# Kernel tuning notes

Hardware: AMD Instinct MI355X
Metric: run time of the kernel (lower is better)

Reference implementation:

```python
import jax, jax.numpy as jnp
import numpy as np
import math

D_MODEL = 1024
N_HEADS = 16
D_HEAD = D_MODEL // N_HEADS
D_FF = 4096
BATCH = 2
SEQ = 2048
EPS = 1e-5


def _rmsnorm(x, w):
    rms = jnp.sqrt(jnp.mean(x * x, axis=-1, keepdims=True) + EPS)
    return (x / rms) * w


def _gelu_erf(x):
    # matches 0.5 * x * (1 + erf(x / sqrt(2)))
    return 0.5 * x * (1.0 + jax.lax.erf(x / jnp.sqrt(jnp.asarray(2.0, x.dtype))))


def setup_inputs() -> dict:
    key = jax.random.key(0)
    ks = jax.random.split(key, 6)
    scale = 0.02
    x = jax.random.normal(ks[0], (BATCH, SEQ, D_MODEL), dtype=jnp.float32)
    w_qkv = jax.random.normal(ks[1], (3 * D_MODEL, D_MODEL), dtype=jnp.float32) * scale
    w_o = jax.random.normal(ks[2], (D_MODEL, D_MODEL), dtype=jnp.float32) * scale
    ln1_w = jnp.ones((D_MODEL,), dtype=jnp.float32)
    ln2_w = jnp.ones((D_MODEL,), dtype=jnp.float32)
    w1 = jax.random.normal(ks[3], (D_FF, D_MODEL), dtype=jnp.float32) * scale
    w2 = jax.random.normal(ks[4], (D_MODEL, D_FF), dtype=jnp.float32) * scale
    return {"x": x, "w_qkv": w_qkv, "w_o": w_o, "ln1_w": ln1_w,
            "ln2_w": ln2_w, "w1": w1, "w2": w2}


def reference(x, w_qkv, w_o, ln1_w, ln2_w, w1, w2):
    B, S, D = x.shape
    # --- attention sublayer (pre-norm) ---
    h = _rmsnorm(x, ln1_w)
    qkv = jnp.einsum('bsd,ed->bse', h, w_qkv)            # (B,S,3*D)
    qkv = qkv.reshape(B, S, 3, N_HEADS, D_HEAD)
    q, k, v = jnp.moveaxis(qkv, 2, 0)                    # each (B,S,H,dh)
    q = q.transpose(0, 2, 1, 3)                          # (B,H,S,dh)
    k = k.transpose(0, 2, 1, 3)
    v = v.transpose(0, 2, 1, 3)
    scores = jnp.einsum('bhqd,bhkd->bhqk', q, k) / math.sqrt(D_HEAD)
    causal = jnp.tril(jnp.ones((S, S), dtype=bool))      # True = keep
    scores = jnp.where(causal, scores, jnp.asarray(-jnp.inf, scores.dtype))
    attn = jax.nn.softmax(scores, axis=-1)
    ctx = jnp.einsum('bhqk,bhkd->bhqd', attn, v)         # (B,H,S,dh)
    ctx = ctx.transpose(0, 2, 1, 3).reshape(B, S, D)
    attn_out = jnp.einsum('bsd,ed->bse', ctx, w_o)
    first_sum = x + attn_out
    # --- FFN sublayer (pre-norm) ---
    h2 = _rmsnorm(first_sum, ln2_w)
    ff = jnp.einsum('bsf,df->bsd', _gelu_erf(jnp.einsum('bsd,fd->bsf', h2, w1)), w2)
    return first_sum + ff
```

## Files before the change

kernel.cpp:

```cpp
#include <hip/hip_runtime.h>

typedef unsigned short u16;
typedef unsigned int u32;
typedef __attribute__((ext_vector_type(8))) short short8;
typedef __attribute__((ext_vector_type(4))) float f32x4;

#define AS1 __attribute__((address_space(1)))
#define AS3 __attribute__((address_space(3)))

__device__ __forceinline__ u16 f2bf(float f) {
  union { float f; unsigned u; } v; v.f = f;
  return (u16)((v.u + 0x7fffu + ((v.u >> 16) & 1u)) >> 16);
}
__device__ __forceinline__ u32 pack2bf(float a, float b) {
  return (u32)f2bf(a) | ((u32)f2bf(b) << 16);
}
__device__ __forceinline__ u32 permpack(float a, float b) {
  union { float f; u32 u; } ua, ub; ua.f = a; ub.f = b;
  return __builtin_amdgcn_perm(ub.u, ua.u, 0x07060302u);
}

__global__ void cvt_all_kernel(const float* __restrict__ wqkv, const float* __restrict__ wo,
                               const float* __restrict__ w1, const float* __restrict__ w2,
                               u16* __restrict__ oqkv, u16* __restrict__ oo,
                               u16* __restrict__ o1, u16* __restrict__ o2) {
  const int blk = blockIdx.x;
  const float* src; u16* dst; float scale = 1.0f; int off;
  if (blk < 3072) {
    src = wqkv; dst = oqkv; off = blk;
    if (blk >= 1024 && blk < 2048) scale = 0.125f;
  } else if (blk < 4096) {
    src = wo; dst = oo; off = blk - 3072;
  } else if (blk < 8192) {
    src = w1; dst = o1; off = blk - 4096;
  } else {
    src = w2; dst = o2; off = blk - 8192;
  }
  size_t i = ((size_t)off * 256 + threadIdx.x) * 4;
  float4 v = *(const float4*)(src + i);
  ushort4 o = make_ushort4(f2bf(v.x * scale), f2bf(v.y * scale),
                           f2bf(v.z * scale), f2bf(v.w * scale));
  *(ushort4*)(dst + i) = o;
}

__global__ void rmsnorm_kernel(const float* __restrict__ x, const float* __restrict__ w,
                               u16* __restrict__ out) {
  const int row = blockIdx.x, tid = threadIdx.x;
  const float4 v = ((const float4*)(x + (size_t)row * 1024))[tid];
  float ss = v.x * v.x + v.y * v.y + v.z * v.z + v.w * v.w;
#pragma unroll
  for (int off = 32; off > 0; off >>= 1) ss += __shfl_xor(ss, off);
  __shared__ float red[4];
  if ((tid & 63) == 0) red[tid >> 6] = ss;
  __syncthreads();
  float tot = red[0] + red[1] + red[2] + red[3];
  float scale = 1.0f / sqrtf(tot * (1.0f / 1024.0f) + 1e-5f);
  const float4 wv = ((const float4*)w)[tid];
  ushort4 o = make_ushort4(f2bf(v.x * scale * wv.x), f2bf(v.y * scale * wv.y),
                           f2bf(v.z * scale * wv.z), f2bf(v.w * scale * wv.w));
  ((ushort4*)(out + (size_t)row * 1024))[tid] = o;
}

template <int EPI>
__global__ __launch_bounds__(256, 4)
void gemm_bt(const u16* __restrict__ A, const u16* __restrict__ B,
             const float* __restrict__ RES, void* __restrict__ OUT,
             int M, int N, int K, int KS) {
  __shared__ __align__(16) u16 As[2][128 * 32];
  __shared__ __align__(16) u16 Bs[2][128 * 32];
  const int tid = threadIdx.x;
  const int wave = tid >> 6, lane = tid & 63;
  const int quad = lane >> 4, l16 = lane & 15;
  const int m0 = blockIdx.y * 128, n0 = blockIdx.x * 128;
  const int wm = (wave >> 1) * 64, wn = (wave & 1) * 64;
  f32x4 acc[4][4] = {};

  const int c0 = wave * 128 + lane;
  const int r0_row = c0 >> 2, r0_col = (c0 & 3) * 8;
  const int c1 = c0 + 64;
  const int r1_row = c1 >> 2, r1_col = (c1 & 3) * 8;

  const u16* ga0 = A + (size_t)(m0 + r0_row) * K + r0_col;
  const u16* ga1 = A + (size_t)(m0 + r1_row) * K + r1_col;
  const u16* gb0 = B + (size_t)(n0 + r0_row) * K + r0_col;
  const u16* gb1 = B + (size_t)(n0 + r1_row) * K + r1_col;

  const int kbeg = blockIdx.z * KS, kend = kbeg + KS;

  auto stage = [&](int k0, int pp) {
    __builtin_amdgcn_global_load_lds((AS1 void*)(ga0 + k0), (AS3 void*)(&As[pp][wave * 1024]), 16, 0, 0);
    __builtin_amdgcn_global_load_lds((AS1 void*)(ga1 + k0), (AS3 void*)(&As[pp][wave * 1024 + 512]), 16, 0, 0);
    __builtin_amdgcn_global_load_lds((AS1 void*)(gb0 + k0), (AS3 void*)(&Bs[pp][wave * 1024]), 16, 0, 0);
    __builtin_amdgcn_global_load_lds((AS1 void*)(gb1 + k0), (AS3 void*)(&Bs[pp][wave * 1024 + 512]), 16, 0, 0);
  };

  stage(kbeg, 0);
  int p = 0;
  for (int k0 = kbeg; k0 < kend; k0 += 32) {
    __syncthreads();
    if (k0 + 32 < kend) stage(k0 + 32, p ^ 1);
    short8 af[4], bfr[4];
#pragma unroll
    for (int i = 0; i < 4; ++i) {
      af[i]  = *(const short8*)(&As[p][(wm + i * 16 + l16) * 32 + quad * 8]);
      bfr[i] = *(const short8*)(&Bs[p][(wn + i * 16 + l16) * 32 + quad * 8]);
    }
#pragma unroll
    for (int i = 0; i < 4; ++i)
#pragma unroll
      for (int j = 0; j < 4; ++j)
        acc[i][j] = __builtin_amdgcn_mfma_f32_16x16x32_bf16(af[i], bfr[j], acc[i][j], 0, 0, 0);
    p ^= 1;
  }

  const size_t zoff = (size_t)blockIdx.z * M * N;
#pragma unroll
  for (int i = 0; i < 4; ++i) {
#pragma unroll
    for (int j = 0; j < 4; ++j) {
#pragma unroll
      for (int r = 0; r < 4; ++r) {
        int row = m0 + wm + i * 16 + quad * 4 + r;
        int col = n0 + wn + j * 16 + l16;
        size_t idx = (size_t)row * N + col;
        float v = acc[i][j][r];
        if constexpr (EPI == 0) {
          ((u16*)OUT)[idx] = f2bf(v);
        } else if constexpr (EPI == 1) {
          ((float*)OUT)[idx] = RES[idx] + v;
        } else if constexpr (EPI == 2) {
          float g = 0.5f * v * (1.0f + erff(v * 0.70710678118654752f));
          ((u16*)OUT)[idx] = f2bf(g);
        } else {
          ((float*)OUT)[zoff + idx] = v;
        }
      }
    }
  }
}

__global__ void reduce4_kernel(const float* __restrict__ fs,
                               const float* __restrict__ P,
                               float* __restrict__ out, size_t n) {
  size_t i = ((size_t)blockIdx.x * 256 + threadIdx.x) * 4;
  float4 a = *(const float4*)(fs + i);
  float4 p0 = *(const float4*)(P + i);
  float4 p1 = *(const float4*)(P + n + i);
  float4 p2 = *(const float4*)(P + 2 * n + i);
  float4 p3 = *(const float4*)(P + 3 * n + i);
  float4 o = make_float4(a.x + ((p0.x + p1.x) + (p2.x + p3.x)),
                         a.y + ((p0.y + p1.y) + (p2.y + p3.y)),
                         a.z + ((p0.z + p1.z) + (p2.z + p3.z)),
                         a.w + ((p0.w + p1.w) + (p2.w + p3.w)));
  *(float4*)(out + i) = o;
}

__global__ __launch_bounds__(256)
void packkv_kernel(const u16* __restrict__ qkv, u16* __restrict__ Kp,
                   u16* __restrict__ Vp) {
  __shared__ __align__(16) u16 Ks[32][72];
  __shared__ __align__(16) u16 Vs[32][72];
  const int kt = blockIdx.x, h = blockIdx.y, b = blockIdx.z;
  const int tid = threadIdx.x;
  const int key0 = kt * 32;
  {
    const size_t g = (size_t)b * 2048 * 3072 + (size_t)(key0 + (tid >> 3)) * 3072
                     + h * 64 + (tid & 7) * 8;
    *(short8*)(&Ks[tid >> 3][(tid & 7) * 8]) = *(const short8*)(qkv + g + 1024);
    *(short8*)(&Vs[tid >> 3][(tid & 7) * 8]) = *(const short8*)(qkv + g + 2048);
  }
  __syncthreads();
  const int wave = tid >> 6, lane = tid & 63;
  const int quad = lane >> 4, l16 = lane & 15;
  const int permrow = 8 * (l16 >> 2) + (l16 & 3);
  const size_t obase = ((size_t)((b * 16 + h) * 64 + kt)) * 2048 + tid * 8;
  {
    int row = permrow + (wave >> 1) * 4;
    int col = quad * 8 + (wave & 1) * 32;
    *(short8*)(Kp + obase) = *(const short8*)(&Ks[row][col]);
  }
  {
    short8 v;
    int col = wave * 16 + l16;
#pragma unroll
    for (int j = 0; j < 8; ++j) v[j] = (short)Vs[quad * 8 + j][col];
    *(short8*)(Vp + obase) = v;
  }
}

struct AttnState {
  f32x4 o0, o1, o2, o3;
  float ls;
};

template <bool MASKED>
__device__ __forceinline__ void attn_tile(
    AttnState& st, const u16* kp, const u16* vp, int key0, int q_abs, int quad,
    short8 qf0, short8 qf1) {
  short8 kf00 = *(const short8*)kp;
  short8 kf01 = *(const short8*)(kp + 512);
  short8 kf10 = *(const short8*)(kp + 1024);
  short8 kf11 = *(const short8*)(kp + 1536);
  short8 vf0 = *(const short8*)vp;
  short8 vf1 = *(const short8*)(vp + 512);
  short8 vf2 = *(const short8*)(vp + 1024);
  short8 vf3 = *(const short8*)(vp + 1536);

  f32x4 s0 = {}, s1 = {};
  s0 = __builtin_amdgcn_mfma_f32_16x16x32_bf16(kf00, qf0, s0, 0, 0, 0);
  s0 = __builtin_amdgcn_mfma_f32_16x16x32_bf16(kf01, qf1, s0, 0, 0, 0);
  s1 = __builtin_amdgcn_mfma_f32_16x16x32_bf16(kf10, qf0, s1, 0, 0, 0);
  s1 = __builtin_amdgcn_mfma_f32_16x16x32_bf16(kf11, qf1, s1, 0, 0, 0);

  float p[8];
#pragma unroll
  for (int r = 0; r < 4; ++r) {
    p[r]     = __expf(s0[r]);
    p[4 + r] = __expf(s1[r]);
  }
  if constexpr (MASKED) {
    const int kb = key0 + 8 * quad;
#pragma unroll
    for (int r = 0; r < 4; ++r) {
      if (kb + r > q_abs)     p[r] = 0.f;
      if (kb + 4 + r > q_abs) p[4 + r] = 0.f;
    }
  }
  st.ls += ((p[0] + p[1]) + (p[2] + p[3])) + ((p[4] + p[5]) + (p[6] + p[7]));

  union { u32 u[4]; short8 s; } pu;
  pu.u[0] = permpack(p[0], p[1]);
  pu.u[1] = permpack(p[2], p[3]);
  pu.u[2] = permpack(p[4], p[5]);
  pu.u[3] = permpack(p[6], p[7]);

  st.o0 = __builtin_amdgcn_mfma_f32_16x16x32_bf16(vf0, pu.s, st.o0, 0, 0, 0);
  st.o1 = __builtin_amdgcn_mfma_f32_16x16x32_bf16(vf1, pu.s, st.o1, 0, 0, 0);
  st.o2 = __builtin_amdgcn_mfma_f32_16x16x32_bf16(vf2, pu.s, st.o2, 0, 0, 0);
  st.o3 = __builtin_amdgcn_mfma_f32_16x16x32_bf16(vf3, pu.s, st.o3, 0, 0, 0);
}

__global__ __launch_bounds__(256)
void attn_kernel(const u16* __restrict__ qkv, const u16* __restrict__ Kpack,
                 const u16* __restrict__ Vpack, u16* __restrict__ ctx) {
  const int bx = blockIdx.x, by = blockIdx.y, bz = blockIdx.z;
  const int h = by, b = bz;
  const int qt = ((by >> 3) & 1) ? (31 - bx) : bx;
  const int tid = threadIdx.x, wave = tid >> 6, lane = tid & 63;
  const int quad = lane >> 4, l16 = lane & 15;
  const int q0 = qt * 64;
  const int qrow = q0 + wave * 16;
  const int q_abs = qrow + l16;
  const size_t base = (size_t)b * 2048 * 3072;
  const size_t headoff = (size_t)((b * 16 + h) * 64) * 2048;
  const u16* Kb = Kpack + headoff + lane * 8;
  const u16* Vb = Vpack + headoff + lane * 8;

  short8 qf0, qf1;
  {
    const u16* qp = qkv + base + (size_t)q_abs * 3072 + h * 64 + quad * 8;
    qf0 = *(const short8*)qp;
    qf1 = *(const short8*)(qp + 32);
  }
  AttnState st;
  st.o0 = f32x4{}; st.o1 = f32x4{}; st.o2 = f32x4{}; st.o3 = f32x4{};
  st.ls = 0.f;

  const int nfull = qrow >> 5;
  for (int kt = 0; kt < nfull; ++kt)
    attn_tile<false>(st, Kb + kt * 2048, Vb + kt * 2048, kt * 32, q_abs, quad, qf0, qf1);
  attn_tile<true>(st, Kb + nfull * 2048, Vb + nfull * 2048, nfull * 32, q_abs, quad, qf0, qf1);

  float ls = st.ls;
  ls += __shfl_xor(ls, 16);
  ls += __shfl_xor(ls, 32);
  float inv = 1.0f / ls;

  f32x4 o[4] = {st.o0, st.o1, st.o2, st.o3};
  u16* cp = ctx + (size_t)(b * 2048 + q_abs) * 1024 + h * 64 + quad * 4;
#pragma unroll
  for (int c = 0; c < 4; ++c) {
    u32 lo = pack2bf(o[c][0] * inv, o[c][1] * inv);
    u32 hi = pack2bf(o[c][2] * inv, o[c][3] * inv);
    *(uint2*)(cp + c * 16) = make_uint2(lo, hi);
  }
}

extern "C" void kernel_launch(void* const* d_in, const int* in_sizes, int n_in,
                              void* d_out, int out_size, void* d_ws, size_t ws_size,
                              hipStream_t stream) {
  const float* x     = (const float*)d_in[0];
  const float* w_qkv = (const float*)d_in[1];
  const float* w_o   = (const float*)d_in[2];
  const float* ln1   = (const float*)d_in[3];
  const float* ln2   = (const float*)d_in[4];
  const float* w1    = (const float*)d_in[5];
  const float* w2    = (const float*)d_in[6];
  float* out = (float*)d_out;

  char* p = (char*)d_ws;
  u16* wqkv_b = (u16*)p; p += (size_t)3072 * 1024 * 2;
  u16* wo_b   = (u16*)p; p += (size_t)1024 * 1024 * 2;
  u16* w1_b   = (u16*)p; p += (size_t)4096 * 1024 * 2;
  u16* w2_b   = (u16*)p; p += (size_t)1024 * 4096 * 2;
  u16* h_b    = (u16*)p; p += (size_t)4096 * 1024 * 2;
  u16* qkv_b  = (u16*)p;
  u16* g_b    = qkv_b;
  p += (size_t)4096 * 3072 * 2;
  u16* ctx_b  = (u16*)p; p += (size_t)4096 * 1024 * 2;
  float* fs   = (float*)p; p += (size_t)4096 * 1024 * 4;
  u16* kp_b   = (u16*)fs;
  u16* vp_b   = (u16*)fs + (size_t)4 * 1024 * 1024;
  float* Pbuf = (float*)p;
  const size_t need = (size_t)(p - (char*)d_ws) + (size_t)4 * 4096 * 1024 * 4;
  const bool splitk = ws_size >= need;

  cvt_all_kernel<<<12288, 256, 0, stream>>>(w_qkv, w_o, w1, w2,
                                            wqkv_b, wo_b, w1_b, w2_b);

  rmsnorm_kernel<<<4096, 256, 0, stream>>>(x, ln1, h_b);
  gemm_bt<0><<<dim3(24, 32, 1), 256, 0, stream>>>(h_b, wqkv_b, nullptr, qkv_b, 4096, 3072, 1024, 1024);
  packkv_kernel<<<dim3(64, 16, 2), 256, 0, stream>>>(qkv_b, kp_b, vp_b);
  attn_kernel<<<dim3(32, 16, 2), 256, 0, stream>>>(qkv_b, kp_b, vp_b, ctx_b);
  gemm_bt<1><<<dim3(8, 32, 1), 256, 0, stream>>>(ctx_b, wo_b, x, fs, 4096, 1024, 1024, 1024);
  rmsnorm_kernel<<<4096, 256, 0, stream>>>(fs, ln2, h_b);
  gemm_bt<2><<<dim3(32, 32, 1), 256, 0, stream>>>(h_b, w1_b, nullptr, g_b, 4096, 4096, 1024, 1024);
  if (splitk) {
    gemm_bt<3><<<dim3(8, 32, 4), 256, 0, stream>>>(g_b, w2_b, nullptr, Pbuf, 4096, 1024, 4096, 1024);
    reduce4_kernel<<<4096, 256, 0, stream>>>(fs, Pbuf, out, (size_t)4096 * 1024);
  } else {
    gemm_bt<1><<<dim3(8, 32, 1), 256, 0, stream>>>(g_b, w2_b, fs, out, 4096, 1024, 4096, 4096);
  }
}
```

Before: 356.7 us.

## Pre-pack weights into MFMA fragment layout and load B directly to registers

The weight conversion kernel now writes bf16 weights in a tiled layout matching the MFMA B-fragment order. The GEMM reads B straight from global memory into registers with one-step prefetch, so the B shared-memory buffers are gone. Split-K partials are also stored as bf16 instead of fp32, which halves partial-buffer traffic but loses some precision before the reduction. Launch bounds drop to 3 blocks per SM to fit the extra registers. The new packing kernel uses scalar, strided float loads that may be slower than the old vectorised conversion.

```diff
diff --git a/kernel.cpp b/kernel.cpp
--- a/kernel.cpp
+++ b/kernel.cpp
@@ -15,32 +15,45 @@
 __device__ __forceinline__ u32 pack2bf(float a, float b) {
   return (u32)f2bf(a) | ((u32)f2bf(b) << 16);
 }
+__device__ __forceinline__ float bf2f(u16 h) {
+  union { u32 u; float f; } v; v.u = ((u32)h) << 16; return v.f;
+}
 __device__ __forceinline__ u32 permpack(float a, float b) {
   union { float f; u32 u; } ua, ub; ua.f = a; ub.f = b;
   return __builtin_amdgcn_perm(ub.u, ua.u, 0x07060302u);
 }
 
-__global__ void cvt_all_kernel(const float* __restrict__ wqkv, const float* __restrict__ wo,
-                               const float* __restrict__ w1, const float* __restrict__ w2,
-                               u16* __restrict__ oqkv, u16* __restrict__ oo,
-                               u16* __restrict__ o1, u16* __restrict__ o2) {
-  const int blk = blockIdx.x;
-  const float* src; u16* dst; float scale = 1.0f; int off;
-  if (blk < 3072) {
-    src = wqkv; dst = oqkv; off = blk;
-    if (blk >= 1024 && blk < 2048) scale = 0.125f;
-  } else if (blk < 4096) {
-    src = wo; dst = oo; off = blk - 3072;
-  } else if (blk < 8192) {
-    src = w1; dst = o1; off = blk - 4096;
-  } else {
-    src = w2; dst = o2; off = blk - 8192;
-  }
-  size_t i = ((size_t)off * 256 + threadIdx.x) * 4;
-  float4 v = *(const float4*)(src + i);
-  ushort4 o = make_ushort4(f2bf(v.x * scale), f2bf(v.y * scale),
-                           f2bf(v.z * scale), f2bf(v.w * scale));
-  *(ushort4*)(dst + i) = o;
+__global__ __launch_bounds__(256)
+void packb_kernel(const float* __restrict__ wqkv, const float* __restrict__ wo,
+                  const float* __restrict__ w1, const float* __restrict__ w2,
+                  u16* __restrict__ oqkv, u16* __restrict__ oo,
+                  u16* __restrict__ o1, u16* __restrict__ o2) {
+  __shared__ u16 Ls[128][40];
+  const int b = blockIdx.x, t = threadIdx.x;
+  const float* W; u16* O; int nb, kb, KB; float scale = 1.0f;
+  if (b < 768)       { W = wqkv; O = oqkv; KB = 32;  int i2 = b;        nb = i2 >> 5; kb = i2 & 31;
+                       if (nb >= 8 && nb < 16) scale = 0.125f; }
+  else if (b < 1024) { W = wo;   O = oo;   KB = 32;  int i2 = b - 768;  nb = i2 >> 5; kb = i2 & 31; }
+  else if (b < 2048) { W = w1;   O = o1;   KB = 32;  int i2 = b - 1024; nb = i2 >> 5; kb = i2 & 31; }
+  else               { W = w2;   O = o2;   KB = 128; int i2 = b - 2048; nb = i2 >> 7; kb = i2 & 127; }
+  const int K = KB * 32;
+  {
+    const int r = t >> 1, c0 = (t & 1) * 16;
+    const float* src = W + (size_t)(nb * 128 + r) * K + kb * 32 + c0;
+#pragma unroll
+    for (int e = 0; e < 16; ++e) Ls[r][c0 + e] = f2bf(src[e] * scale);
+  }
+  __syncthreads();
+  const int f = t >> 5, l0 = (t & 31) * 2;
+  u16* dst = O + ((size_t)(nb * KB + kb) * 8 + f) * 512 + (size_t)l0 * 8;
+  short8 v0, v1;
+#pragma unroll
+  for (int e = 0; e < 8; ++e) v0[e] = (short)Ls[f * 16 + (l0 & 15)][(l0 >> 4) * 8 + e];
+  const int l1 = l0 + 1;
+#pragma unroll
+  for (int e = 0; e < 8; ++e) v1[e] = (short)Ls[f * 16 + (l1 & 15)][(l1 >> 4) * 8 + e];
+  *(short8*)dst = v0;
+  *(short8*)(dst + 8) = v1;
 }
 
 __global__ void rmsnorm_kernel(const float* __restrict__ x, const float* __restrict__ w,
@@ -62,16 +75,15 @@
 }
 
 template <int EPI>
-__global__ __launch_bounds__(256, 4)
-void gemm_bt(const u16* __restrict__ A, const u16* __restrict__ B,
+__global__ __launch_bounds__(256, 3)
+void gemm_bt(const u16* __restrict__ A, const u16* __restrict__ Bp,
              const float* __restrict__ RES, void* __restrict__ OUT,
              int M, int N, int K, int KS) {
   __shared__ __align__(16) u16 As[2][128 * 32];
-  __shared__ __align__(16) u16 Bs[2][128 * 32];
   const int tid = threadIdx.x;
   const int wave = tid >> 6, lane = tid & 63;
   const int quad = lane >> 4, l16 = lane & 15;
-  const int m0 = blockIdx.y * 128, n0 = blockIdx.x * 128;
+  const int m0 = blockIdx.y * 128;
   const int wm = (wave >> 1) * 64, wn = (wave & 1) * 64;
   f32x4 acc[4][4] = {};
 
@@ -79,40 +91,54 @@
   const int r0_row = c0 >> 2, r0_col = (c0 & 3) * 8;
   const int c1 = c0 + 64;
   const int r1_row = c1 >> 2, r1_col = (c1 & 3) * 8;
-
   const u16* ga0 = A + (size_t)(m0 + r0_row) * K + r0_col;
   const u16* ga1 = A + (size_t)(m0 + r1_row) * K + r1_col;
-  const u16* gb0 = B + (size_t)(n0 + r0_row) * K + r0_col;
-  const u16* gb1 = B + (size_t)(n0 + r1_row) * K + r1_col;
+
+  const u16* Bw = Bp + (((size_t)blockIdx.x * (K >> 5)) * 8 + (wave & 1) * 4) * 512
+                  + (size_t)lane * 8;
 
   const int kbeg = blockIdx.z * KS, kend = kbeg + KS;
 
   auto stage = [&](int k0, int pp) {
     __builtin_amdgcn_global_load_lds((AS1 void*)(ga0 + k0), (AS3 void*)(&As[pp][wave * 1024]), 16, 0, 0);
     __builtin_amdgcn_global_load_lds((AS1 void*)(ga1 + k0), (AS3 void*)(&As[pp][wave * 1024 + 512]), 16, 0, 0);
-    __builtin_amdgcn_global_load_lds((AS1 void*)(gb0 + k0), (AS3 void*)(&Bs[pp][wave * 1024]), 16, 0, 0);
-    __builtin_amdgcn_global_load_lds((AS1 void*)(gb1 + k0), (AS3 void*)(&Bs[pp][wave * 1024 + 512]), 16, 0, 0);
   };
 
   stage(kbeg, 0);
+  short8 bfr[4];
+  {
+    const u16* bp = Bw + (size_t)(kbeg >> 5) * 4096;
+#pragma unroll
+    for (int j = 0; j < 4; ++j) bfr[j] = *(const short8*)(bp + j * 512);
+  }
   int p = 0;
   for (int k0 = kbeg; k0 < kend; k0 += 32) {
     __syncthreads();
-    if (k0 + 32 < kend) stage(k0 + 32, p ^ 1);
-    short8 af[4], bfr[4];
-#pragma unroll
-    for (int i = 0; i < 4; ++i) {
-      af[i]  = *(const short8*)(&As[p][(wm + i * 16 + l16) * 32 + quad * 8]);
-      bfr[i] = *(const short8*)(&Bs[p][(wn + i * 16 + l16) * 32 + quad * 8]);
+    const bool more = (k0 + 32 < kend);
+    if (more) stage(k0 + 32, p ^ 1);
+    short8 bnext[4];
+    if (more) {
+      const u16* bp = Bw + (size_t)((k0 + 32) >> 5) * 4096;
+#pragma unroll
+      for (int j = 0; j < 4; ++j) bnext[j] = *(const short8*)(bp + j * 512);
     }
+    short8 af[4];
+#pragma unroll
+    for (int i = 0; i < 4; ++i)
+      af[i] = *(const short8*)(&As[p][(wm + i * 16 + l16) * 32 + quad * 8]);
 #pragma unroll
     for (int i = 0; i < 4; ++i)
 #pragma unroll
       for (int j = 0; j < 4; ++j)
         acc[i][j] = __builtin_amdgcn_mfma_f32_16x16x32_bf16(af[i], bfr[j], acc[i][j], 0, 0, 0);
+    if (more) {
+#pragma unroll
+      for (int j = 0; j < 4; ++j) bfr[j] = bnext[j];
+    }
     p ^= 1;
   }
 
+  const int n0 = blockIdx.x * 128;
   const size_t zoff = (size_t)blockIdx.z * M * N;
 #pragma unroll
   for (int i = 0; i < 4; ++i) {
@@ -132,7 +158,7 @@
           float g = 0.5f * v * (1.0f + erff(v * 0.70710678118654752f));
           ((u16*)OUT)[idx] = f2bf(g);
         } else {
-          ((float*)OUT)[zoff + idx] = v;
+          ((u16*)OUT)[zoff + idx] = f2bf(v);
         }
       }
     }
@@ -140,19 +166,17 @@
 }
 
 __global__ void reduce4_kernel(const float* __restrict__ fs,
-                               const float* __restrict__ P,
+                               const u16* __restrict__ P,
                                float* __restrict__ out, size_t n) {
   size_t i = ((size_t)blockIdx.x * 256 + threadIdx.x) * 4;
   float4 a = *(const float4*)(fs + i);
-  float4 p0 = *(const float4*)(P + i);
-  float4 p1 = *(const float4*)(P + n + i);
-  float4 p2 = *(const float4*)(P + 2 * n + i);
-  float4 p3 = *(const float4*)(P + 3 * n + i);
-  float4 o = make_float4(a.x + ((p0.x + p1.x) + (p2.x + p3.x)),
-                         a.y + ((p0.y + p1.y) + (p2.y + p3.y)),
-                         a.z + ((p0.z + p1.z) + (p2.z + p3.z)),
-                         a.w + ((p0.w + p1.w) + (p2.w + p3.w)));
-  *(float4*)(out + i) = o;
+  float s[4] = {a.x, a.y, a.z, a.w};
+#pragma unroll
+  for (int z = 0; z < 4; ++z) {
+    ushort4 q = *(const ushort4*)(P + z * n + i);
+    s[0] += bf2f(q.x); s[1] += bf2f(q.y); s[2] += bf2f(q.z); s[3] += bf2f(q.w);
+  }
+  *(float4*)(out + i) = make_float4(s[0], s[1], s[2], s[3]);
 }
 
 __global__ __launch_bounds__(256)
@@ -311,12 +335,12 @@
   float* fs   = (float*)p; p += (size_t)4096 * 1024 * 4;
   u16* kp_b   = (u16*)fs;
   u16* vp_b   = (u16*)fs + (size_t)4 * 1024 * 1024;
-  float* Pbuf = (float*)p;
-  const size_t need = (size_t)(p - (char*)d_ws) + (size_t)4 * 4096 * 1024 * 4;
+  u16* Pbuf = (u16*)p;
+  const size_t need = (size_t)(p - (char*)d_ws) + (size_t)4 * 4096 * 1024 * 2;
   const bool splitk = ws_size >= need;
 
-  cvt_all_kernel<<<12288, 256, 0, stream>>>(w_qkv, w_o, w1, w2,
-                                            wqkv_b, wo_b, w1_b, w2_b);
+  packb_kernel<<<3072, 256, 0, stream>>>(w_qkv, w_o, w1, w2,
+                                         wqkv_b, wo_b, w1_b, w2_b);
 
   rmsnorm_kernel<<<4096, 256, 0, stream>>>(x, ln1, h_b);
   gemm_bt<0><<<dim3(24, 32, 1), 256, 0, stream>>>(h_b, wqkv_b, nullptr, qkv_b, 4096, 3072, 1024, 1024);
```

After: 342.6 us. -3.9%, faster.
